# Optimization experiments

Measured on AMD Instinct MI355X. Metric: run time of the kernel, lower is better.

Reference implementation:

```python
import jax, jax.numpy as jnp
import numpy as np

N_EMBD = 768
N_HEAD = 8
HEAD_DIM = N_EMBD // N_HEAD


def setup_inputs() -> dict:
    key = jax.random.key(0)
    k1, k2, k3 = jax.random.split(key, 3)
    B, T, C = 8, 1024, N_EMBD
    x = jax.random.normal(k1, (B, T, C), dtype=jnp.float32)
    # nn.Linear(C, 3C, bias=False): store as [C, 3C] so y = x @ W
    W_attn = jax.random.normal(k2, (C, 3 * C), dtype=jnp.float32) * (1.0 / np.sqrt(C))
    W_proj = jax.random.normal(k3, (C, C), dtype=jnp.float32) * (1.0 / np.sqrt(C))
    return {"x": x, "W_attn": W_attn, "W_proj": W_proj}


def reference(x, W_attn, W_proj):
    B, T, C = x.shape
    qkv = x @ W_attn                      # [B,T,3C]
    q, k, v = jnp.split(qkv, 3, axis=2)
    # [B,T,C] -> [B,H,T,D]
    def heads(t):
        return t.reshape(B, T, N_HEAD, HEAD_DIM).transpose(0, 2, 1, 3)
    q, k, v = heads(q), heads(k), heads(v)
    scale = 1.0 / np.sqrt(HEAD_DIM)
    att = jnp.einsum('bhtd,bhsd->bhts', q, k) * scale  # [B,H,T,T]
    causal = jnp.tril(jnp.ones((T, T), dtype=bool))
    att = jnp.where(causal[None, None], att, -jnp.inf)
    att = jax.nn.softmax(att, axis=-1)
    y = jnp.einsum('bhts,bhsd->bhtd', att, v)          # [B,H,T,D]
    y = y.transpose(0, 2, 1, 3).reshape(B, T, C)
    return y @ W_proj
```

## Files before the change

kernel.cpp:

```cpp
#include <hip/hip_runtime.h>
#include <stdint.h>

#define Bz 8
#define Tz 1024
#define Cz 768
#define Hz 8
#define Dz 96
#define BHz 64
#define Kz 768

typedef __bf16 bf16x8 __attribute__((ext_vector_type(8)));
typedef unsigned short u16x8 __attribute__((ext_vector_type(8)));
typedef float f32x4 __attribute__((ext_vector_type(4)));

__device__ __forceinline__ unsigned short f2bf(float f) {
  union { float f; unsigned int u; } v; v.f = f;
  unsigned int u = v.u;
  return (unsigned short)((u + 0x7fffu + ((u >> 16) & 1u)) >> 16);
}

#if defined(__has_builtin)
#if __has_builtin(__builtin_amdgcn_exp2f)
#define EXP2(x) __builtin_amdgcn_exp2f(x)
#endif
#endif
#ifndef EXP2
#define EXP2(x) __expf((x) * 0.6931471805599453f)
#endif

typedef const __attribute__((address_space(1))) void* gas_ptr;
typedef __attribute__((address_space(3))) void* las_ptr;
__device__ __forceinline__ void gl16(const void* g, void* l) {
  __builtin_amdgcn_global_load_lds((gas_ptr)g, (las_ptr)l, 16, 0, 0);
}

__global__ __launch_bounds__(256) void cast_f32_bf16(const float* __restrict__ in,
                                                     unsigned short* __restrict__ out) {
  int i = (blockIdx.x * 256 + threadIdx.x) * 4;
  float4 v = *(const float4*)(in + i);
  union { unsigned short s[4]; uint2 u; } o;
  o.s[0] = f2bf(v.x); o.s[1] = f2bf(v.y); o.s[2] = f2bf(v.z); o.s[3] = f2bf(v.w);
  *(uint2*)(out + i) = o.u;
}

__global__ __launch_bounds__(256) void transpose_cast(const float* __restrict__ in,
                                                      unsigned short* __restrict__ out,
                                                      int R, int Cc) {
  __shared__ unsigned short t[64][72];
  int bx = blockIdx.x * 64;
  int by = blockIdx.y * 64;
  int tid = threadIdx.x;
#pragma unroll
  for (int i = 0; i < 16; i++) {
    int idx = tid + i * 256;
    int r = idx >> 6, c = idx & 63;
    t[c][r] = f2bf(in[(by + r) * Cc + bx + c]);
  }
  __syncthreads();
#pragma unroll
  for (int i = 0; i < 16; i++) {
    int idx = tid + i * 256;
    int r = idx >> 6, c = idx & 63;
    out[(bx + r) * R + by + c] = t[r][c];
  }
}

template <int MODE>
__global__ __launch_bounds__(256)
void gemm128(const unsigned short* __restrict__ A,
             const unsigned short* __restrict__ Bt,
             unsigned short* __restrict__ obf,
             float* __restrict__ of32) {
  __shared__ unsigned short Asm[128 * 32];
  __shared__ unsigned short Bsm[128 * 32];
  const int tid = threadIdx.x;
  const int wave = tid >> 6, lane = tid & 63;
  const int quad = lane >> 4, l16 = lane & 15;
  const int bm = blockIdx.x, bn = blockIdx.y;
  const int wm = (wave >> 1) * 64, wn = (wave & 1) * 64;

  f32x4 zero = {0.f, 0.f, 0.f, 0.f};
  f32x4 acc[4][4];
#pragma unroll
  for (int i = 0; i < 4; i++)
#pragma unroll
    for (int j = 0; j < 4; j++) acc[i][j] = zero;

  const int rr = lane >> 2, c8 = (lane & 3) * 8;
  const unsigned short* Ag0 = A + (size_t)(bm * 128 + wave * 32 + rr) * Kz + c8;
  const unsigned short* Ag1 = Ag0 + 16 * Kz;
  const unsigned short* Bg0 = Bt + (size_t)(bn * 128 + wave * 32 + rr) * Kz + c8;
  const unsigned short* Bg1 = Bg0 + 16 * Kz;
  unsigned short* lA0 = &Asm[wave * 1024];
  unsigned short* lA1 = lA0 + 512;
  unsigned short* lB0 = &Bsm[wave * 1024];
  unsigned short* lB1 = lB0 + 512;

  for (int k0 = 0; k0 < Kz; k0 += 32) {
    __syncthreads();
    gl16(Ag0 + k0, lA0);
    gl16(Ag1 + k0, lA1);
    gl16(Bg0 + k0, lB0);
    gl16(Bg1 + k0, lB1);
    __syncthreads();
    bf16x8 af[4], bfr[4];
#pragma unroll
    for (int mi = 0; mi < 4; mi++)
      af[mi] = *(const bf16x8*)&Asm[(wm + mi * 16 + l16) * 32 + quad * 8];
#pragma unroll
    for (int ni = 0; ni < 4; ni++)
      bfr[ni] = *(const bf16x8*)&Bsm[(wn + ni * 16 + l16) * 32 + quad * 8];
#pragma unroll
    for (int mi = 0; mi < 4; mi++)
#pragma unroll
      for (int ni = 0; ni < 4; ni++)
        acc[mi][ni] = __builtin_amdgcn_mfma_f32_16x16x32_bf16(af[mi], bfr[ni], acc[mi][ni], 0, 0, 0);
  }

#pragma unroll
  for (int mi = 0; mi < 4; mi++) {
    int row = bm * 128 + wm + mi * 16 + quad * 4;
    if (MODE == 0) {
      int b = row >> 10;
      int t = row & 1023;
#pragma unroll
      for (int ni = 0; ni < 4; ni++) {
        int col = bn * 128 + wn + ni * 16 + l16;
        int which = col / 768;
        int cc = col - which * 768;
        int h = cc / 96;
        int d = cc - h * 96;
        if (which == 2) {
          int base = ((2 * 64 + b * 8 + h) * 96 + d) * 1024 + t;
          union { unsigned short s[4]; uint2 u; } o;
#pragma unroll
          for (int r = 0; r < 4; r++) o.s[r] = f2bf(acc[mi][ni][r]);
          *(uint2*)(obf + base) = o.u;
        } else {
          int base = ((which * 64 + b * 8 + h) * 1024 + t) * 96 + d;
#pragma unroll
          for (int r = 0; r < 4; r++) obf[base + r * 96] = f2bf(acc[mi][ni][r]);
        }
      }
    } else {
#pragma unroll
      for (int ni = 0; ni < 4; ni++) {
        int col = bn * 128 + wn + ni * 16 + l16;
#pragma unroll
        for (int r = 0; r < 4; r++) of32[(row + r) * 768 + col] = acc[mi][ni][r];
      }
    }
  }
}

__global__ __launch_bounds__(256, 3)
void attn(const unsigned short* __restrict__ qkv, unsigned short* __restrict__ y) {
  const int bh = blockIdx.x;
  const int by = blockIdx.y;
  const int q0 = (15 - by) * 64;
  const int tid = threadIdx.x;
  const int wave = tid >> 6, lane = tid & 63;
  const int quad = lane >> 4, l16 = lane & 15;
  const int qw0 = q0 + wave * 16;
  const int b = bh >> 3, h = bh & 7;

  const unsigned short* Qh = qkv + bh * Tz * Dz;
  const unsigned short* Kh = qkv + (BHz + bh) * Tz * Dz;
  const unsigned short* Vt = qkv + 2 * BHz * Tz * Dz + bh * Dz * Tz;

  __shared__ unsigned short Vsm[96 * 136];
  __shared__ unsigned short Psm[4 * 16 * 136];
  unsigned short* Pw = Psm + wave * 16 * 136;

  const int vd = tid >> 4;
  const int vc = tid & 15;

  bf16x8 aq[3];
#pragma unroll
  for (int kd = 0; kd < 3; kd++)
    aq[kd] = *(const bf16x8*)(Qh + (qw0 + l16) * Dz + kd * 32 + quad * 8);

  f32x4 zero = {0.f, 0.f, 0.f, 0.f};
  f32x4 acc_o[6];
#pragma unroll
  for (int i = 0; i < 6; i++) acc_o[i] = zero;
  const float NEG = -__builtin_inff();
  float mrow[4], lrow[4];
#pragma unroll
  for (int r = 0; r < 4; r++) { mrow[r] = NEG; lrow[r] = 0.f; }
  const float cs = 0.14724538519872735f;

  const int s_last = (q0 >> 7) << 7;
  for (int s0 = 0; s0 <= s_last; s0 += 128) {
    u16x8 vreg[6];
#pragma unroll
    for (int g = 0; g < 6; g++)
      vreg[g] = *(const u16x8*)(Vt + (g * 16 + vd) * Tz + s0 + vc * 8);

    const int srem = qw0 + 15 - s0;
    const int nlim = min(7, srem >> 4);
    const int klim = min(3, srem >> 5);

    f32x4 sacc[8];
#pragma unroll
    for (int ni = 0; ni < 8; ni++) {
      if (ni <= nlim) {
        sacc[ni] = zero;
#pragma unroll
        for (int kd = 0; kd < 3; kd++) {
          bf16x8 bk = *(const bf16x8*)(Kh + (s0 + ni * 16 + l16) * Dz + kd * 32 + quad * 8);
          sacc[ni] = __builtin_amdgcn_mfma_f32_16x16x32_bf16(aq[kd], bk, sacc[ni], 0, 0, 0);
        }
      }
    }

    float rmax[4] = {NEG, NEG, NEG, NEG};
#pragma unroll
    for (int ni = 0; ni < 8; ni++) {
      if (ni <= nlim) {
        if (s0 + ni * 16 + 15 > qw0) {
          const int t_base = qw0 + quad * 4;
          const int s_abs = s0 + ni * 16 + l16;
#pragma unroll
          for (int r = 0; r < 4; r++)
            if (s_abs > t_base + r) sacc[ni][r] = NEG;
        }
#pragma unroll
        for (int r = 0; r < 4; r++) rmax[r] = fmaxf(rmax[r], sacc[ni][r]);
      }
    }
#pragma unroll
    for (int r = 0; r < 4; r++)
#pragma unroll
      for (int sh = 1; sh < 16; sh <<= 1)
        rmax[r] = fmaxf(rmax[r], __shfl_xor(rmax[r], sh));

    int ok = 1;
#pragma unroll
    for (int r = 0; r < 4; r++) ok &= (rmax[r] <= mrow[r] + 54.0f) ? 1 : 0;
    if (!__all(ok)) {
#pragma unroll
      for (int r = 0; r < 4; r++) {
        float mnew = fmaxf(mrow[r], rmax[r]);
        float alpha = EXP2((mrow[r] - mnew) * cs);
        mrow[r] = mnew;
        lrow[r] *= alpha;
#pragma unroll
        for (int di = 0; di < 6; di++) acc_o[di][r] *= alpha;
      }
    }

    float nmc[4];
#pragma unroll
    for (int r = 0; r < 4; r++) nmc[r] = -mrow[r] * cs;
    float rsum[4] = {0.f, 0.f, 0.f, 0.f};
#pragma unroll
    for (int ni = 0; ni < 8; ni++) {
      if (ni <= nlim) {
#pragma unroll
        for (int r = 0; r < 4; r++) {
          float p = EXP2(fmaf(sacc[ni][r], cs, nmc[r]));
          rsum[r] += p;
          Pw[(quad * 4 + r) * 136 + ni * 16 + l16] = f2bf(p);
        }
      }
    }
#pragma unroll
    for (int r = 0; r < 4; r++) lrow[r] += rsum[r];

    if (nlim < 7 && !(nlim & 1)) {
      const int zc = (nlim + 1) * 16 + l16;
#pragma unroll
      for (int r = 0; r < 4; r++) Pw[(quad * 4 + r) * 136 + zc] = 0;
    }

    __syncthreads();
#pragma unroll
    for (int g = 0; g < 6; g++)
      *(u16x8*)&Vsm[(g * 16 + vd) * 136 + vc * 8] = vreg[g];
    __syncthreads();

#pragma unroll
    for (int kc = 0; kc < 4; kc++) {
      if (kc <= klim) {
        bf16x8 ap = *(const bf16x8*)&Pw[l16 * 136 + kc * 32 + quad * 8];
#pragma unroll
        for (int di = 0; di < 6; di++) {
          bf16x8 bv = *(const bf16x8*)&Vsm[(di * 16 + l16) * 136 + kc * 32 + quad * 8];
          acc_o[di] = __builtin_amdgcn_mfma_f32_16x16x32_bf16(ap, bv, acc_o[di], 0, 0, 0);
        }
      }
    }
  }

#pragma unroll
  for (int r = 0; r < 4; r++) {
#pragma unroll
    for (int sh = 1; sh < 16; sh <<= 1)
      lrow[r] += __shfl_xor(lrow[r], sh);
    float linv = 1.f / lrow[r];
    int t = qw0 + quad * 4 + r;
#pragma unroll
    for (int di = 0; di < 6; di++) {
      int d = di * 16 + l16;
      y[(b * Tz + t) * Cz + h * Dz + d] = f2bf(acc_o[di][r] * linv);
    }
  }
}

#define OFF_XB   0u
#define OFF_WAT  12582912u
#define OFF_WPT  16121856u
#define OFF_QKV  17301504u
#define OFF_Y    55050240u

extern "C" void kernel_launch(void* const* d_in, const int* in_sizes, int n_in,
                              void* d_out, int out_size, void* d_ws, size_t ws_size,
                              hipStream_t stream) {
  const float* x  = (const float*)d_in[0];
  const float* Wa = (const float*)d_in[1];
  const float* Wp = (const float*)d_in[2];
  float* out = (float*)d_out;
  uint8_t* ws = (uint8_t*)d_ws;
  unsigned short* xb  = (unsigned short*)(ws + OFF_XB);
  unsigned short* Wat = (unsigned short*)(ws + OFF_WAT);
  unsigned short* Wpt = (unsigned short*)(ws + OFF_WPT);
  unsigned short* qkv = (unsigned short*)(ws + OFF_QKV);
  unsigned short* y   = (unsigned short*)(ws + OFF_Y);

  cast_f32_bf16<<<6144, 256, 0, stream>>>(x, xb);
  transpose_cast<<<dim3(36, 12), 256, 0, stream>>>(Wa, Wat, 768, 2304);
  transpose_cast<<<dim3(12, 12), 256, 0, stream>>>(Wp, Wpt, 768, 768);
  gemm128<0><<<dim3(64, 18), 256, 0, stream>>>(xb, Wat, qkv, nullptr);
  attn<<<dim3(64, 16), 256, 0, stream>>>(qkv, y);
  gemm128<1><<<dim3(64, 6), 256, 0, stream>>>(y, Wpt, nullptr, out);
}
```

Before: 206.3 us.

## Compute transposed S tile and build P operand in registers via shuffles

The attention kernel now computes S^T with swapped MFMA operands, so each lane owns one query row. That turns the row max and sum reductions into two cross-quad shuffles instead of sixteen. P is packed to bf16 with v_cvt_pk_bf16_f32 and rearranged into the A-operand layout with lane shuffles, which removes the per-wave P shared-memory buffer and its LDS round trip. Freeing that LDS allows raising the occupancy hint from 3 to 4 blocks, at the cost of extra shuffle and select instructions per k-chunk and possible register pressure.

New measurement: 217.6 us. 1.05x slower.

```diff
diff --git a/kernel.cpp b/kernel.cpp
--- a/kernel.cpp
+++ b/kernel.cpp
@@ -17,6 +17,12 @@
   union { float f; unsigned int u; } v; v.f = f;
   unsigned int u = v.u;
   return (unsigned short)((u + 0x7fffu + ((u >> 16) & 1u)) >> 16);
+}
+
+__device__ __forceinline__ unsigned int cvtpk(float a, float b) {
+  unsigned int r;
+  asm("v_cvt_pk_bf16_f32 %0, %1, %2" : "=v"(r) : "v"(a), "v"(b));
+  return r;
 }
 
 #if defined(__has_builtin)
@@ -153,7 +159,7 @@
   }
 }
 
-__global__ __launch_bounds__(256, 3)
+__global__ __launch_bounds__(256, 4)
 void attn(const unsigned short* __restrict__ qkv, unsigned short* __restrict__ y) {
   const int bh = blockIdx.x;
   const int by = blockIdx.y;
@@ -169,8 +175,6 @@
   const unsigned short* Vt = qkv + 2 * BHz * Tz * Dz + bh * Dz * Tz;
 
   __shared__ unsigned short Vsm[96 * 136];
-  __shared__ unsigned short Psm[4 * 16 * 136];
-  unsigned short* Pw = Psm + wave * 16 * 136;
 
   const int vd = tid >> 4;
   const int vc = tid & 15;
@@ -185,10 +189,9 @@
 #pragma unroll
   for (int i = 0; i < 6; i++) acc_o[i] = zero;
   const float NEG = -__builtin_inff();
-  float mrow[4], lrow[4];
-#pragma unroll
-  for (int r = 0; r < 4; r++) { mrow[r] = NEG; lrow[r] = 0.f; }
+  float mrow = NEG, lrow = 0.f;
   const float cs = 0.14724538519872735f;
+  const int t_abs = qw0 + l16;
 
   const int s_last = (q0 >> 7) << 7;
   for (int s0 = 0; s0 <= s_last; s0 += 128) {
@@ -209,70 +212,62 @@
 #pragma unroll
         for (int kd = 0; kd < 3; kd++) {
           bf16x8 bk = *(const bf16x8*)(Kh + (s0 + ni * 16 + l16) * Dz + kd * 32 + quad * 8);
-          sacc[ni] = __builtin_amdgcn_mfma_f32_16x16x32_bf16(aq[kd], bk, sacc[ni], 0, 0, 0);
+          sacc[ni] = __builtin_amdgcn_mfma_f32_16x16x32_bf16(bk, aq[kd], sacc[ni], 0, 0, 0);
         }
       }
     }
 
-    float rmax[4] = {NEG, NEG, NEG, NEG};
+    float rmx[4] = {NEG, NEG, NEG, NEG};
 #pragma unroll
     for (int ni = 0; ni < 8; ni++) {
       if (ni <= nlim) {
         if (s0 + ni * 16 + 15 > qw0) {
-          const int t_base = qw0 + quad * 4;
-          const int s_abs = s0 + ni * 16 + l16;
+          const int s_base = s0 + ni * 16 + quad * 4;
 #pragma unroll
           for (int r = 0; r < 4; r++)
-            if (s_abs > t_base + r) sacc[ni][r] = NEG;
+            if (s_base + r > t_abs) sacc[ni][r] = NEG;
         }
 #pragma unroll
-        for (int r = 0; r < 4; r++) rmax[r] = fmaxf(rmax[r], sacc[ni][r]);
-      }
-    }
-#pragma unroll
-    for (int r = 0; r < 4; r++)
-#pragma unroll
-      for (int sh = 1; sh < 16; sh <<= 1)
-        rmax[r] = fmaxf(rmax[r], __shfl_xor(rmax[r], sh));
-
-    int ok = 1;
-#pragma unroll
-    for (int r = 0; r < 4; r++) ok &= (rmax[r] <= mrow[r] + 54.0f) ? 1 : 0;
+        for (int r = 0; r < 4; r++) rmx[r] = fmaxf(rmx[r], sacc[ni][r]);
+      }
+    }
+    float rmax = fmaxf(fmaxf(rmx[0], rmx[1]), fmaxf(rmx[2], rmx[3]));
+    rmax = fmaxf(rmax, __shfl_xor(rmax, 16));
+    rmax = fmaxf(rmax, __shfl_xor(rmax, 32));
+
+    int ok = (rmax <= mrow + 54.0f) ? 1 : 0;
     if (!__all(ok)) {
-#pragma unroll
-      for (int r = 0; r < 4; r++) {
-        float mnew = fmaxf(mrow[r], rmax[r]);
-        float alpha = EXP2((mrow[r] - mnew) * cs);
-        mrow[r] = mnew;
-        lrow[r] *= alpha;
-#pragma unroll
-        for (int di = 0; di < 6; di++) acc_o[di][r] *= alpha;
-      }
-    }
-
-    float nmc[4];
-#pragma unroll
-    for (int r = 0; r < 4; r++) nmc[r] = -mrow[r] * cs;
-    float rsum[4] = {0.f, 0.f, 0.f, 0.f};
+      float mnew = fmaxf(mrow, rmax);
+      float alpha = EXP2((mrow - mnew) * cs);
+      mrow = mnew;
+      lrow *= alpha;
+      float av[4];
+#pragma unroll
+      for (int r = 0; r < 4; r++) av[r] = __shfl(alpha, quad * 4 + r);
+#pragma unroll
+      for (int di = 0; di < 6; di++)
+#pragma unroll
+        for (int r = 0; r < 4; r++) acc_o[di][r] *= av[r];
+    }
+
+    const float nmc = -mrow * cs;
+    float rs[4] = {0.f, 0.f, 0.f, 0.f};
+    unsigned int pk[8][2];
 #pragma unroll
     for (int ni = 0; ni < 8; ni++) {
       if (ni <= nlim) {
-#pragma unroll
-        for (int r = 0; r < 4; r++) {
-          float p = EXP2(fmaf(sacc[ni][r], cs, nmc[r]));
-          rsum[r] += p;
-          Pw[(quad * 4 + r) * 136 + ni * 16 + l16] = f2bf(p);
-        }
-      }
-    }
-#pragma unroll
-    for (int r = 0; r < 4; r++) lrow[r] += rsum[r];
-
-    if (nlim < 7 && !(nlim & 1)) {
-      const int zc = (nlim + 1) * 16 + l16;
-#pragma unroll
-      for (int r = 0; r < 4; r++) Pw[(quad * 4 + r) * 136 + zc] = 0;
-    }
+        float p0 = EXP2(fmaf(sacc[ni][0], cs, nmc));
+        float p1 = EXP2(fmaf(sacc[ni][1], cs, nmc));
+        float p2 = EXP2(fmaf(sacc[ni][2], cs, nmc));
+        float p3 = EXP2(fmaf(sacc[ni][3], cs, nmc));
+        rs[0] += p0; rs[1] += p1; rs[2] += p2; rs[3] += p3;
+        pk[ni][0] = cvtpk(p0, p1);
+        pk[ni][1] = cvtpk(p2, p3);
+      } else {
+        pk[ni][0] = 0u; pk[ni][1] = 0u;
+      }
+    }
+    lrow += (rs[0] + rs[1]) + (rs[2] + rs[3]);
 
     __syncthreads();
 #pragma unroll
@@ -283,27 +278,43 @@
 #pragma unroll
     for (int kc = 0; kc < 4; kc++) {
       if (kc <= klim) {
-        bf16x8 ap = *(const bf16x8*)&Pw[l16 * 136 + kc * 32 + quad * 8];
+        const unsigned int a0 = pk[2 * kc][0], a1 = pk[2 * kc][1];
+        const unsigned int b0 = pk[2 * kc + 1][0], b1 = pk[2 * kc + 1][1];
+        const unsigned int s0w = (quad < 2) ? b0 : a0;
+        const unsigned int s1w = (quad < 2) ? b1 : a1;
+        const unsigned int u0 = (unsigned int)__shfl_xor((int)s0w, 32);
+        const unsigned int u1 = (unsigned int)__shfl_xor((int)s1w, 32);
+        const unsigned int t0w = (quad == 0 || quad == 3) ? u0 : ((quad == 1) ? a0 : b0);
+        const unsigned int t1w = (quad == 0 || quad == 3) ? u1 : ((quad == 1) ? a1 : b1);
+        const unsigned int r0 = (unsigned int)__shfl_xor((int)t0w, 16);
+        const unsigned int r1 = (unsigned int)__shfl_xor((int)t1w, 16);
+        union { unsigned int w[4]; bf16x8 v; } ap;
+        ap.w[0] = (quad == 0) ? a0 : ((quad == 2) ? u0 : r0);
+        ap.w[1] = (quad == 0) ? a1 : ((quad == 2) ? u1 : r1);
+        ap.w[2] = (quad == 0) ? r0 : ((quad == 1) ? u0 : ((quad == 2) ? r0 : b0));
+        ap.w[3] = (quad == 0) ? r1 : ((quad == 1) ? u1 : ((quad == 2) ? r1 : b1));
 #pragma unroll
         for (int di = 0; di < 6; di++) {
           bf16x8 bv = *(const bf16x8*)&Vsm[(di * 16 + l16) * 136 + kc * 32 + quad * 8];
-          acc_o[di] = __builtin_amdgcn_mfma_f32_16x16x32_bf16(ap, bv, acc_o[di], 0, 0, 0);
+          acc_o[di] = __builtin_amdgcn_mfma_f32_16x16x32_bf16(ap.v, bv, acc_o[di], 0, 0, 0);
         }
       }
     }
   }
 
+  lrow += __shfl_xor(lrow, 16);
+  lrow += __shfl_xor(lrow, 32);
+  float linv = 1.f / lrow;
+  float lv[4];
+#pragma unroll
+  for (int r = 0; r < 4; r++) lv[r] = __shfl(linv, quad * 4 + r);
 #pragma unroll
   for (int r = 0; r < 4; r++) {
-#pragma unroll
-    for (int sh = 1; sh < 16; sh <<= 1)
-      lrow[r] += __shfl_xor(lrow[r], sh);
-    float linv = 1.f / lrow[r];
     int t = qw0 + quad * 4 + r;
 #pragma unroll
     for (int di = 0; di < 6; di++) {
       int d = di * 16 + l16;
-      y[(b * Tz + t) * Cz + h * Dz + d] = f2bf(acc_o[di][r] * linv);
+      y[(b * Tz + t) * Cz + h * Dz + d] = f2bf(acc_o[di][r] * lv[r]);
     }
   }
 }
```
